# Kernel optimization log

Measured on AMD Instinct MI355X. Metric: run time of the kernel, lower is better.

Reference implementation:

```python
import jax, jax.numpy as jnp
import numpy as np

N = 50000      # nodes
E = 800000     # edges
D = 200        # in_dim = hid_dim
R = 230        # num_rels
B = 100        # bdd bases -> submat = D // B = 2
S = D // B     # submatrix size (2)


def setup_inputs() -> dict:
    key = jax.random.key(0)
    ks = jax.random.split(key, 16)
    node_feat = jax.random.normal(ks[0], (N, D), dtype=jnp.float32)
    dynamic_emb = jax.random.normal(ks[1], (N, 1, D), dtype=jnp.float32)
    src = jax.random.randint(ks[2], (E,), 0, N, dtype=jnp.int32)
    dst = jax.random.randint(ks[3], (E,), 0, N, dtype=jnp.int32)
    etypes = jax.random.randint(ks[4], (E,), 0, R, dtype=jnp.int32)
    # BDD relational weights per layer: [R, B, S, S]
    w1 = jax.random.normal(ks[5], (R, B, S, S), dtype=jnp.float32) * 0.1
    loop_w1 = jax.random.normal(ks[6], (D, D), dtype=jnp.float32) * 0.05
    b1 = jnp.zeros((D,), dtype=jnp.float32)
    w2 = jax.random.normal(ks[7], (R, B, S, S), dtype=jnp.float32) * 0.1
    loop_w2 = jax.random.normal(ks[8], (D, D), dtype=jnp.float32) * 0.05
    b2 = jnp.zeros((D,), dtype=jnp.float32)
    # single-layer vanilla RNN (tanh) params
    W_ih = jax.random.normal(ks[9], (D, D), dtype=jnp.float32) * 0.05
    W_hh = jax.random.normal(ks[10], (D, D), dtype=jnp.float32) * 0.05
    b_ih = jnp.zeros((D,), dtype=jnp.float32)
    b_hh = jnp.zeros((D,), dtype=jnp.float32)
    return {"node_feat": node_feat, "dynamic_emb": dynamic_emb,
            "src": src, "dst": dst, "etypes": etypes,
            "w1": w1, "loop_w1": loop_w1, "b1": b1,
            "w2": w2, "loop_w2": loop_w2, "b2": b2,
            "W_ih": W_ih, "W_hh": W_hh, "b_ih": b_ih, "b_hh": b_hh}


def _rel_graph_conv_bdd(x, src, dst, etypes, edge_norm, w, loop_w, b):
    # gather source feats and apply per-edge-type block-diagonal transform
    xs = x[src].reshape(E, B, S)                     # [E, B, S]
    msg = jnp.einsum('ebi,ebio->ebo', xs, w[etypes]) # [E, B, S]
    msg = msg.reshape(E, D) * edge_norm              # edge-norm scaling
    agg = jax.ops.segment_sum(msg, dst, num_segments=N)  # scatter-add to dst
    return agg + x @ loop_w + b                      # self-loop + bias


def reference(node_feat, dynamic_emb, src, dst, etypes,
              w1, loop_w1, b1, w2, loop_w2, b2,
              W_ih, W_hh, b_ih, b_hh):
    # edge_norm = dst node norm = 1 / in-degree
    deg = jax.ops.segment_sum(jnp.ones((E,), jnp.float32), dst, num_segments=N)
    node_norm = jnp.where(deg > 0, 1.0 / jnp.maximum(deg, 1.0), 0.0)
    edge_norm = node_norm[dst][:, None]              # [E, 1]

    # RGCN layer 1 (tanh activation), layer 2 (no activation); dropout=eval
    h = _rel_graph_conv_bdd(node_feat, src, dst, etypes, edge_norm, w1, loop_w1, b1)
    h = jnp.tanh(h)
    h = _rel_graph_conv_bdd(h, src, dst, etypes, edge_norm, w2, loop_w2, b2)

    # single-step vanilla RNN: hn = tanh(x W_ih^T + b_ih + h0 W_hh^T + b_hh)
    h0 = dynamic_emb[:, 0, :]                        # [N, D]
    hn = jnp.tanh(h @ W_ih.T + b_ih + h0 @ W_hh.T + b_hh)
    return hn[:, None, :]                            # [N, 1, D]
```

## Files before the change

kernel.cpp:

```cpp
#include <hip/hip_runtime.h>

#define N_NODES 50000
#define N_EDGES 800000
#define DIM     200
#define NBLK    100
#define NRELS   230
#define NB_SCAN 196
#define KPAD    224
#define KPN     256
#define NROWPAD 50048
#define NFRAG8  (8 * 14 * 64)
#define EPADMAX (N_EDGES + 3 * N_NODES + 16)
#define DUMMYROW 50000

typedef __attribute__((ext_vector_type(8)))  short short8;
typedef __attribute__((ext_vector_type(16))) float f32x16;

__device__ __forceinline__ unsigned short f2bf(float f) {
    unsigned u = __float_as_uint(f);
    u += 0x7fffu + ((u >> 16) & 1u);
    return (unsigned short)(u >> 16);
}

__device__ __forceinline__ float bflo(unsigned u) { return __uint_as_float(u << 16); }
__device__ __forceinline__ float bfhi(unsigned u) { return __uint_as_float(u & 0xffff0000u); }
__device__ __forceinline__ float b2f(unsigned short u) { return __uint_as_float((unsigned)u << 16); }

__device__ __forceinline__ float tanh_fast(float x) {
    float xa = fminf(fmaxf(x, -15.0f), 15.0f);
    float e = __expf(2.0f * xa);
    return (e - 1.0f) / (e + 1.0f);
}

__device__ __forceinline__ int uread(int v, int l) {
    return __builtin_amdgcn_readlane(v, l);
}

#if __has_builtin(__builtin_amdgcn_fdot2_f32_bf16)
typedef __bf16 bf16x2 __attribute__((ext_vector_type(2)));
__device__ __forceinline__ float dot2bf(unsigned a, unsigned b, float c) {
    return __builtin_amdgcn_fdot2_f32_bf16(
        __builtin_bit_cast(bf16x2, a), __builtin_bit_cast(bf16x2, b), c, false);
}
#define CMP4(XU, WU)                                                    \
    { m0 = dot2bf(XU.x, WU.x, m0); m1 = dot2bf(XU.x, WU.y, m1);         \
      m2 = dot2bf(XU.y, WU.z, m2); m3 = dot2bf(XU.y, WU.w, m3); }
#else
#define CMP4(XU, WU)                                                    \
    { float x0 = bflo(XU.x), x1 = bfhi(XU.x);                           \
      float x2 = bflo(XU.y), x3 = bfhi(XU.y);                           \
      m0 += x0 * bflo(WU.x) + x1 * bfhi(WU.x);                          \
      m1 += x0 * bflo(WU.y) + x1 * bfhi(WU.y);                          \
      m2 += x2 * bflo(WU.z) + x3 * bfhi(WU.z);                          \
      m3 += x2 * bflo(WU.w) + x3 * bfhi(WU.w); }
#endif

#define SWZ5(rr, off) ((unsigned)((rr) * 512 + (off)) ^ ((unsigned)((rr) & 15) << 4))
#define SWZH(rr, off) ((unsigned)((rr) * 256 + (off)) ^ ((unsigned)((rr) & 15) << 4))

#define FD_A (2 * NROWPAD * 28)
#define FD_B N_EDGES
#define FD_TOTAL (FD_A + FD_B)

__global__ void featdeg(const float* __restrict__ x, const float* __restrict__ de,
                        unsigned short* __restrict__ xb, unsigned short* __restrict__ h0b,
                        const int* __restrict__ dst, int* __restrict__ degi) {
    int idx = blockIdx.x * blockDim.x + threadIdx.x;
    if (idx < FD_A) {
        const int HALF = NROWPAD * 28;
        const float* src = (idx < HALF) ? x : de;
        unsigned short* o = (idx < HALF) ? xb : h0b;
        int j = (idx < HALF) ? idx : idx - HALF;
        int row = j / 28, c8 = j % 28;
        uint4 pk = {0, 0, 0, 0};
        if (row < N_NODES && c8 < 25) {
            const float* p = src + (size_t)row * DIM + c8 * 8;
            float4 a = *(const float4*)p;
            float4 b = *(const float4*)(p + 4);
            pk.x = (unsigned)f2bf(a.x) | ((unsigned)f2bf(a.y) << 16);
            pk.y = (unsigned)f2bf(a.z) | ((unsigned)f2bf(a.w) << 16);
            pk.z = (unsigned)f2bf(b.x) | ((unsigned)f2bf(b.y) << 16);
            pk.w = (unsigned)f2bf(b.z) | ((unsigned)f2bf(b.w) << 16);
        }
        *(uint4*)(o + (size_t)j * 8) = pk;
        return;
    }
    idx -= FD_A;
    if (idx < FD_B) atomicAdd(&degi[dst[idx]], 1);
}

#define PS_C (2 * NRELS * NBLK)
#define PS_D (3 * NFRAG8)
#define PS_E ((DIM + 1) * DIM)
#define PS_TOTAL (PS_C + PS_D + PS_E)

__global__ __launch_bounds__(256) void prep_small(
        const float* __restrict__ w1, const float* __restrict__ w2,
        unsigned short* __restrict__ w1b, unsigned short* __restrict__ w2b,
        const float* __restrict__ lw1, const float* __restrict__ wih,
        const float* __restrict__ whh,
        unsigned short* __restrict__ w1f, unsigned short* __restrict__ wihf,
        unsigned short* __restrict__ whhf,
        const float* __restrict__ lw2, const float* __restrict__ b2,
        const float* __restrict__ b_ih, const float* __restrict__ b_hh,
        float* __restrict__ Mt) {
    int idx = blockIdx.x * blockDim.x + threadIdx.x;
    if (idx < PS_C) {
        const int HALF = NRELS * NBLK;
        const float* w = (idx < HALF) ? w1 : w2;
        unsigned short* o = (idx < HALF) ? w1b : w2b;
        int j = (idx < HALF) ? idx : idx - HALF;
        float4 v = *(const float4*)(w + (size_t)j * 4);
        unsigned c0 = (unsigned)f2bf(v.x) | ((unsigned)f2bf(v.z) << 16);
        unsigned c1 = (unsigned)f2bf(v.y) | ((unsigned)f2bf(v.w) << 16);
        *(uint2*)(o + (size_t)j * 4) = make_uint2(c0, c1);
        return;
    }
    idx -= PS_C;
    if (idx < PS_D) {
        int sec = idx / NFRAG8, f = idx % NFRAG8;
        const float* w = (sec == 0) ? lw1 : (sec == 1) ? wih : whh;
        unsigned short* o = (sec == 0) ? w1f : (sec == 1) ? wihf : whhf;
        int l = f & 63;
        int ks = (f >> 6) % 14;
        int nt = f / (14 * 64);
        int n  = nt * 32 + (l & 31);
        int k0 = ks * 16 + (l >> 5) * 8;
        unsigned short v[8];
        #pragma unroll
        for (int j = 0; j < 8; ++j) {
            int k = k0 + j;
            float val = 0.0f;
            if (n < DIM && k < DIM)
                val = (sec == 0) ? w[k * DIM + n] : w[n * DIM + k];
            v[j] = f2bf(val);
        }
        *(uint4*)(o + (size_t)f * 8) = *(uint4*)v;
        return;
    }
    idx -= PS_D;
    if (idx < PS_E) {
        int k = idx / DIM, n = idx % DIM;
        const float* ar = (k < DIM) ? (lw2 + (size_t)k * DIM) : b2;
        const float* br = wih + (size_t)n * DIM;
        float s0 = 0.f, s1 = 0.f, s2 = 0.f, s3 = 0.f;
        #pragma unroll 5
        for (int q = 0; q < DIM; q += 4) {
            float4 a = *(const float4*)(ar + q);
            float4 b = *(const float4*)(br + q);
            s0 += a.x * b.x; s1 += a.y * b.y; s2 += a.z * b.z; s3 += a.w * b.w;
        }
        float s = (s0 + s1) + (s2 + s3);
        if (k == DIM) s += b_ih[n] + b_hh[n];
        Mt[idx] = s;
    }
}

__global__ __launch_bounds__(256) void scanA(const int* __restrict__ degi,
                                             int* __restrict__ pos, int* __restrict__ cur,
                                             int* __restrict__ bsum) {
    __shared__ int tmp[256];
    int t = threadIdx.x;
    int g = blockIdx.x * 256 + t;
    int d = (g < N_NODES) ? degi[g] : 0;
    int v = (d + 3) & ~3;
    tmp[t] = v;
    __syncthreads();
    for (int off = 1; off < 256; off <<= 1) {
        int xv = (t >= off) ? tmp[t - off] : 0;
        __syncthreads();
        tmp[t] += xv;
        __syncthreads();
    }
    if (g < N_NODES) { int e = tmp[t] - v; pos[g] = e; cur[g] = e; }
    if (t == 255) bsum[blockIdx.x] = tmp[255];
}

__global__ __launch_bounds__(256) void scanC2(int* __restrict__ pos, int* __restrict__ cur,
                                              const int* __restrict__ bsum) {
    __shared__ int tmp[256];
    __shared__ int excl[256];
    int t = threadIdx.x;
    int v = (t < NB_SCAN) ? bsum[t] : 0;
    tmp[t] = v;
    __syncthreads();
    for (int off = 1; off < 256; off <<= 1) {
        int xv = (t >= off) ? tmp[t - off] : 0;
        __syncthreads();
        tmp[t] += xv;
        __syncthreads();
    }
    excl[t] = tmp[t] - v;
    __syncthreads();
    int add = excl[blockIdx.x];
    int g = blockIdx.x * 256 + t;
    if (g < N_NODES) { pos[g] += add; cur[g] += add; }
}

#define M2_A N_EDGES
#define M2_B N_NODES
#define M2_C (NFRAG8 + KPN)
#define M2_TOTAL (M2_A + M2_B + M2_C)

__global__ __launch_bounds__(256) void mega2(
        const int* __restrict__ src, const int* __restrict__ dst,
        const int* __restrict__ et,
        int* __restrict__ cur, const int* __restrict__ pos,
        const int* __restrict__ degi, int* __restrict__ se,
        const float* __restrict__ Mt, unsigned short* __restrict__ Mf,
        float* __restrict__ biasv) {
    int idx = blockIdx.x * blockDim.x + threadIdx.x;
    if (idx < M2_A) {
        int d = dst[idx];
        int slot = atomicAdd(&cur[d], 1);
        se[slot] = src[idx] | (et[idx] << 16);
        return;
    }
    idx -= M2_A;
    if (idx < M2_B) {
        int d = degi[idx];
        if (d > 0) {
            int dp = (d + 3) & ~3;
            int start = pos[idx];
            for (int j = d; j < dp; ++j) se[start + j] = DUMMYROW;
        }
        return;
    }
    idx -= M2_B;
    if (idx < NFRAG8) {
        int l = idx & 63;
        int ks = (idx >> 6) % 14;
        int nt = idx / (14 * 64);
        int n  = nt * 32 + (l & 31);
        int k0 = ks * 16 + (l >> 5) * 8;
        unsigned short v[8];
        #pragma unroll
        for (int j = 0; j < 8; ++j) {
            int k = k0 + j;
            v[j] = f2bf((n < DIM && k < DIM) ? Mt[k * DIM + n] : 0.0f);
        }
        *(uint4*)(Mf + (size_t)idx * 8) = *(uint4*)v;
    } else if (idx < NFRAG8 + KPN) {
        int n = idx - NFRAG8;
        biasv[n] = (n < DIM) ? Mt[DIM * DIM + n] : 0.0f;
    }
}

#define GL(QQ, XU, WU)                                                  \
    { int p_ = uread(sv, (QQ)); int s_ = p_ & 0xffff; int r_ = p_ >> 16;\
      XU = *(const uint2*)(x  + (size_t)s_ * KPAD + xoff);              \
      WU = *(const uint4*)(wb + (size_t)r_ * (NBLK * 4) + woff); }

__global__ __launch_bounds__(256) void gatherB(
        const unsigned short* __restrict__ x,
        const int*   __restrict__ se,
        const int*   __restrict__ pstart,
        const int*   __restrict__ degi,
        const unsigned short* __restrict__ wb,
        unsigned short* __restrict__ agg) {
    int node = (blockIdx.x * blockDim.x + threadIdx.x) >> 6;
    int lane = threadIdx.x & 63;
    if (node >= N_NODES) return;
    int deg = __builtin_amdgcn_readfirstlane(degi[node]);
    const bool act = (lane < 50);
    int cl   = act ? lane : 49;
    int xoff = 4 * cl;
    int woff = 8 * cl;

    if (deg == 0) {
        if (lane < 56) *(uint2*)(agg + (size_t)node * KPAD + 4 * lane) = make_uint2(0u, 0u);
        return;
    }
    int start = __builtin_amdgcn_readfirstlane(pstart[node]);
    int degp  = (deg + 3) & ~3;

    float m0 = 0.f, m1 = 0.f, m2 = 0.f, m3 = 0.f;

    for (int base = 0; base < degp; base += 64) {
        int cnt = degp - base; if (cnt > 64) cnt = 64;
        int sv = se[start + base + (lane < cnt ? lane : cnt - 1)];

        uint2 X0, X1, X2, X3, Y0, Y1, Y2, Y3;
        uint4 W0, W1, W2, W3, V0, V1, V2, V3;
        GL(0, X0, W0); GL(1, X1, W1); GL(2, X2, W2); GL(3, X3, W3);

        for (int q = 0; q < cnt; q += 8) {
            bool l1 = (q + 4 < cnt);
            if (l1) { GL(q + 4, Y0, V0); GL(q + 5, Y1, V1); GL(q + 6, Y2, V2); GL(q + 7, Y3, V3); }
            CMP4(X0, W0); CMP4(X1, W1); CMP4(X2, W2); CMP4(X3, W3);
            if (!l1) break;
            bool l2 = (q + 8 < cnt);
            if (l2) { GL(q + 8, X0, W0); GL(q + 9, X1, W1); GL(q + 10, X2, W2); GL(q + 11, X3, W3); }
            CMP4(Y0, V0); CMP4(Y1, V1); CMP4(Y2, V2); CMP4(Y3, V3);
        }
    }
    float nrm = 1.0f / (float)deg;
    uint2 ov = make_uint2(0u, 0u);
    if (act) {
        ov.x = (unsigned)f2bf(m0 * nrm) | ((unsigned)f2bf(m1 * nrm) << 16);
        ov.y = (unsigned)f2bf(m2 * nrm) | ((unsigned)f2bf(m3 * nrm) << 16);
    }
    if (lane < 56) *(uint2*)(agg + (size_t)node * KPAD + 4 * lane) = ov;
}

__global__ __launch_bounds__(256) void gemm1_kernel(
        unsigned short* xb_hb,
        const unsigned short* __restrict__ agg1,
        const float* __restrict__ b1,
        const unsigned short* __restrict__ w1f) {
    __shared__ __align__(16) unsigned short s_a[32 * KPN];
    int row0 = blockIdx.x * 32;
    int tid = threadIdx.x;
    for (int i = tid; i < 32 * 32; i += 256) {
        int rr = i >> 5, ch = i & 31;
        uint4 v = {0, 0, 0, 0};
        if (ch < 28) v = *(const uint4*)(xb_hb + (size_t)(row0 + rr) * KPAD + ch * 8);
        *(uint4*)((char*)s_a + SWZ5(rr, ch * 16)) = v;
    }
    __syncthreads();

    int l = tid & 63, wv = tid >> 6;
    int rl = l & 31, hl = l >> 5;
    int ntlo = wv * 2;
    const unsigned short* wb = w1f + (size_t)(ntlo * 14) * 512 + l * 8;

    f32x16 acc0 = {}, acc1 = {};
    short8 aC  = *(const short8*)((const char*)s_a + SWZ5(rl, (hl * 8) * 2));
    short8 b0C = *(const short8*)(wb);
    short8 b1C = *(const short8*)(wb + 14 * 512);
    #pragma unroll
    for (int ks = 0; ks < 13; ++ks) {
        short8 aN = {}, b0N = {}, b1N = {};
        if (ks < 12) {
            aN  = *(const short8*)((const char*)s_a + SWZ5(rl, ((ks + 1) * 16 + hl * 8) * 2));
            b0N = *(const short8*)(wb + (ks + 1) * 512);
            b1N = *(const short8*)(wb + 14 * 512 + (ks + 1) * 512);
        }
        acc0 = __builtin_amdgcn_mfma_f32_32x32x16_bf16(aC, b0C, acc0, 0, 0, 0);
        acc1 = __builtin_amdgcn_mfma_f32_32x32x16_bf16(aC, b1C, acc1, 0, 0, 0);
        aC = aN; b0C = b0N; b1C = b1N;
    }
    __syncthreads();

    #pragma unroll
    for (int t = 0; t < 2; ++t) {
        f32x16 ac = t ? acc1 : acc0;
        int gc = (ntlo + t) * 32 + rl;
        if (gc >= KPAD) continue;
        float bias = (gc < DIM) ? b1[gc] : 0.0f;
        #pragma unroll
        for (int r = 0; r < 16; ++r) {
            int gr = row0 + (r & 3) + 8 * (r >> 2) + 4 * hl;
            float v = 0.0f;
            if (gc < DIM && gr < N_NODES)
                v = ac[r] + b2f(agg1[(size_t)gr * KPAD + gc]) + bias;
            xb_hb[(size_t)gr * KPAD + gc] = f2bf(tanh_fast(v));
        }
    }
}

__global__ __launch_bounds__(256) void gemm2_kernel(
        const unsigned short* __restrict__ hb,
        const unsigned short* __restrict__ aggp,
        const unsigned short* __restrict__ h0b,
        const unsigned short* __restrict__ Mf,
        const unsigned short* __restrict__ wihf,
        const unsigned short* __restrict__ whhf,
        const float* __restrict__ biasv,
        float* __restrict__ out) {
    __shared__ __align__(16) unsigned short s_h[32 * 128];
    __shared__ __align__(16) unsigned short s_g[32 * 128];
    __shared__ __align__(16) unsigned short s_e[32 * 128];
    int row0 = blockIdx.x * 32;
    int tid = threadIdx.x;
    int l = tid & 63, wv = tid >> 6;
    int rl = l & 31, hl = l >> 5;
    int ntlo = wv * 2;
    const unsigned short* pm = Mf   + (size_t)(ntlo * 14) * 512 + l * 8;
    const unsigned short* pi = wihf + (size_t)(ntlo * 14) * 512 + l * 8;
    const unsigned short* ph = whhf + (size_t)(ntlo * 14) * 512 + l * 8;

    f32x16 a0 = {}, a1 = {};

    for (int half = 0; half < 2; ++half) {
        for (int i = tid; i < 32 * 14; i += 256) {
            int rr = i / 14, ch = i % 14;
            size_t off = (size_t)(row0 + rr) * KPAD + (half * 14 + ch) * 8;
            unsigned sw = SWZH(rr, ch * 16);
            *(uint4*)((char*)s_h + sw) = *(const uint4*)(hb   + off);
            *(uint4*)((char*)s_g + sw) = *(const uint4*)(aggp + off);
            *(uint4*)((char*)s_e + sw) = *(const uint4*)(h0b  + off);
        }
        __syncthreads();

        const int kbase = half * 7;
        unsigned off0 = SWZH(rl, (hl * 8) * 2);
        short8 hC  = *(const short8*)((const char*)s_h + off0);
        short8 gC  = *(const short8*)((const char*)s_g + off0);
        short8 eC  = *(const short8*)((const char*)s_e + off0);
        short8 m0C = *(const short8*)(pm + kbase * 512);
        short8 m1C = *(const short8*)(pm + 14 * 512 + kbase * 512);
        short8 i0C = *(const short8*)(pi + kbase * 512);
        short8 i1C = *(const short8*)(pi + 14 * 512 + kbase * 512);
        short8 h0C = *(const short8*)(ph + kbase * 512);
        short8 h1C = *(const short8*)(ph + 14 * 512 + kbase * 512);
        #pragma unroll
        for (int ks = 0; ks < 7; ++ks) {
            short8 hN = {}, gN = {}, eN = {};
            short8 m0N = {}, m1N = {}, i0N = {}, i1N = {}, h0N = {}, h1N = {};
            if (ks < 6) {
                unsigned off = SWZH(rl, ((ks + 1) * 16 + hl * 8) * 2);
                hN  = *(const short8*)((const char*)s_h + off);
                gN  = *(const short8*)((const char*)s_g + off);
                eN  = *(const short8*)((const char*)s_e + off);
                int kg = kbase + ks + 1;
                m0N = *(const short8*)(pm + kg * 512);
                m1N = *(const short8*)(pm + 14 * 512 + kg * 512);
                i0N = *(const short8*)(pi + kg * 512);
                i1N = *(const short8*)(pi + 14 * 512 + kg * 512);
                h0N = *(const short8*)(ph + kg * 512);
                h1N = *(const short8*)(ph + 14 * 512 + kg * 512);
            }
            a0 = __builtin_amdgcn_mfma_f32_32x32x16_bf16(hC, m0C, a0, 0, 0, 0);
            a1 = __builtin_amdgcn_mfma_f32_32x32x16_bf16(hC, m1C, a1, 0, 0, 0);
            a0 = __builtin_amdgcn_mfma_f32_32x32x16_bf16(gC, i0C, a0, 0, 0, 0);
            a1 = __builtin_amdgcn_mfma_f32_32x32x16_bf16(gC, i1C, a1, 0, 0, 0);
            a0 = __builtin_amdgcn_mfma_f32_32x32x16_bf16(eC, h0C, a0, 0, 0, 0);
            a1 = __builtin_amdgcn_mfma_f32_32x32x16_bf16(eC, h1C, a1, 0, 0, 0);
            hC = hN; gC = gN; eC = eN;
            m0C = m0N; m1C = m1N; i0C = i0N; i1C = i1N; h0C = h0N; h1C = h1N;
        }
        __syncthreads();
    }

    #pragma unroll
    for (int t = 0; t < 2; ++t) {
        f32x16 oc = t ? a1 : a0;
        int gc = (ntlo + t) * 32 + rl;
        if (gc >= DIM) continue;
        float bias = biasv[gc];
        #pragma unroll
        for (int r = 0; r < 16; ++r) {
            int gr = row0 + (r & 3) + 8 * (r >> 2) + 4 * hl;
            if (gr < N_NODES)
                out[(size_t)gr * DIM + gc] = tanh_fast(oc[r] + bias);
        }
    }
}

extern "C" void kernel_launch(void* const* d_in, const int* in_sizes, int n_in,
                              void* d_out, int out_size, void* d_ws, size_t ws_size,
                              hipStream_t stream) {
    const float* node_feat = (const float*)d_in[0];
    const float* dyn_emb   = (const float*)d_in[1];
    const int*   src       = (const int*)  d_in[2];
    const int*   dst       = (const int*)  d_in[3];
    const int*   etypes    = (const int*)  d_in[4];
    const float* w1        = (const float*)d_in[5];
    const float* loop_w1   = (const float*)d_in[6];
    const float* b1        = (const float*)d_in[7];
    const float* w2        = (const float*)d_in[8];
    const float* loop_w2   = (const float*)d_in[9];
    const float* b2        = (const float*)d_in[10];
    const float* W_ih      = (const float*)d_in[11];
    const float* W_hh      = (const float*)d_in[12];
    const float* b_ih      = (const float*)d_in[13];
    const float* b_hh      = (const float*)d_in[14];
    float* out = (float*)d_out;

    int*   degi = (int*)d_ws;
    int*   pos  = degi + 51200;
    int*   cur  = pos  + 51200;
    int*   bsum = cur  + 51200;
    int*   se   = bsum + 256;
    unsigned short* aggp = (unsigned short*)(se + EPADMAX);
    unsigned short* hb   = aggp + (size_t)NROWPAD * KPAD;
    unsigned short* h0b  = hb   + (size_t)NROWPAD * KPAD;
    unsigned short* w1f  = h0b  + (size_t)NROWPAD * KPAD;
    unsigned short* wihf = w1f  + (size_t)NFRAG8 * 8;
    unsigned short* whhf = wihf + (size_t)NFRAG8 * 8;
    unsigned short* Mf   = whhf + (size_t)NFRAG8 * 8;
    unsigned short* w1b  = Mf   + (size_t)NFRAG8 * 8;
    unsigned short* w2b  = w1b  + (size_t)NRELS * NBLK * 4;
    float* biasv = (float*)(w2b + (size_t)NRELS * NBLK * 4);
    float* Mt    = biasv + KPN;

    hipMemsetAsync(degi, 0, 51200 * sizeof(int), stream);

    featdeg<<<(FD_TOTAL + 255) / 256, 256, 0, stream>>>(
        node_feat, dyn_emb, hb, h0b, dst, degi);
    prep_small<<<(PS_TOTAL + 255) / 256, 256, 0, stream>>>(
        w1, w2, w1b, w2b, loop_w1, W_ih, W_hh, w1f, wihf, whhf,
        loop_w2, b2, b_ih, b_hh, Mt);

    scanA<<<NB_SCAN, 256, 0, stream>>>(degi, pos, cur, bsum);
    scanC2<<<NB_SCAN, 256, 0, stream>>>(pos, cur, bsum);

    mega2<<<(M2_TOTAL + 255) / 256, 256, 0, stream>>>(
        src, dst, etypes, cur, pos, degi, se, Mt, Mf, biasv);

    gatherB<<<(N_NODES * 64 + 255) / 256, 256, 0, stream>>>(
        hb, se, pos, degi, w1b, aggp);
    gemm1_kernel<<<(N_NODES + 31) / 32, 256, 0, stream>>>(
        hb, aggp, b1, w1f);

    gatherB<<<(N_NODES * 64 + 255) / 256, 256, 0, stream>>>(
        hb, se, pos, degi, w2b, aggp);

    gemm2_kernel<<<(N_NODES + 31) / 32, 256, 0, stream>>>(
        hb, aggp, h0b, Mf, wihf, whhf, biasv, out);
}
```

Measured before the change: 333.5 us.

## Record per-edge rank from degree atomics to drop second atomic pass in CSR fill

The degree-count atomicAdd now saves its return value as a per-edge rank, so the CSR scatter in mega2 computes its slot as pos[dst]+rank with no second atomicAdd on a cursor array. Both edge loops now handle 8 edges per thread with vectorised int4 loads, and the feature bf16 conversion is split into its own kernel. The cur array and its writes in the scans are removed. This costs an extra 3.2 MB rank array written and read back, plus one more kernel launch.

```diff
diff --git a/kernel.cpp b/kernel.cpp
--- a/kernel.cpp
+++ b/kernel.cpp
@@ -58,35 +58,45 @@
 #define SWZ5(rr, off) ((unsigned)((rr) * 512 + (off)) ^ ((unsigned)((rr) & 15) << 4))
 #define SWZH(rr, off) ((unsigned)((rr) * 256 + (off)) ^ ((unsigned)((rr) & 15) << 4))
 
-#define FD_A (2 * NROWPAD * 28)
-#define FD_B N_EDGES
-#define FD_TOTAL (FD_A + FD_B)
-
-__global__ void featdeg(const float* __restrict__ x, const float* __restrict__ de,
-                        unsigned short* __restrict__ xb, unsigned short* __restrict__ h0b,
-                        const int* __restrict__ dst, int* __restrict__ degi) {
+__global__ void deg_rank(const int* __restrict__ dst, int* __restrict__ degi,
+                         int* __restrict__ rank) {
     int idx = blockIdx.x * blockDim.x + threadIdx.x;
-    if (idx < FD_A) {
-        const int HALF = NROWPAD * 28;
-        const float* src = (idx < HALF) ? x : de;
-        unsigned short* o = (idx < HALF) ? xb : h0b;
-        int j = (idx < HALF) ? idx : idx - HALF;
-        int row = j / 28, c8 = j % 28;
-        uint4 pk = {0, 0, 0, 0};
-        if (row < N_NODES && c8 < 25) {
-            const float* p = src + (size_t)row * DIM + c8 * 8;
-            float4 a = *(const float4*)p;
-            float4 b = *(const float4*)(p + 4);
-            pk.x = (unsigned)f2bf(a.x) | ((unsigned)f2bf(a.y) << 16);
-            pk.y = (unsigned)f2bf(a.z) | ((unsigned)f2bf(a.w) << 16);
-            pk.z = (unsigned)f2bf(b.x) | ((unsigned)f2bf(b.y) << 16);
-            pk.w = (unsigned)f2bf(b.z) | ((unsigned)f2bf(b.w) << 16);
-        }
-        *(uint4*)(o + (size_t)j * 8) = pk;
-        return;
-    }
-    idx -= FD_A;
-    if (idx < FD_B) atomicAdd(&degi[dst[idx]], 1);
+    if (idx >= N_EDGES / 8) return;
+    int e0 = idx * 8;
+    int4 da = *(const int4*)(dst + e0);
+    int4 db = *(const int4*)(dst + e0 + 4);
+    int r0 = atomicAdd(&degi[da.x], 1);
+    int r1 = atomicAdd(&degi[da.y], 1);
+    int r2 = atomicAdd(&degi[da.z], 1);
+    int r3 = atomicAdd(&degi[da.w], 1);
+    int r4 = atomicAdd(&degi[db.x], 1);
+    int r5 = atomicAdd(&degi[db.y], 1);
+    int r6 = atomicAdd(&degi[db.z], 1);
+    int r7 = atomicAdd(&degi[db.w], 1);
+    *(int4*)(rank + e0)     = make_int4(r0, r1, r2, r3);
+    *(int4*)(rank + e0 + 4) = make_int4(r4, r5, r6, r7);
+}
+
+__global__ void prep_feat2(const float* __restrict__ x, const float* __restrict__ de,
+                           unsigned short* __restrict__ xb, unsigned short* __restrict__ h0b) {
+    const int HALF = NROWPAD * 28;
+    int idx = blockIdx.x * blockDim.x + threadIdx.x;
+    if (idx >= 2 * HALF) return;
+    const float* src = (idx < HALF) ? x : de;
+    unsigned short* o = (idx < HALF) ? xb : h0b;
+    int j = (idx < HALF) ? idx : idx - HALF;
+    int row = j / 28, c8 = j % 28;
+    uint4 pk = {0, 0, 0, 0};
+    if (row < N_NODES && c8 < 25) {
+        const float* p = src + (size_t)row * DIM + c8 * 8;
+        float4 a = *(const float4*)p;
+        float4 b = *(const float4*)(p + 4);
+        pk.x = (unsigned)f2bf(a.x) | ((unsigned)f2bf(a.y) << 16);
+        pk.y = (unsigned)f2bf(a.z) | ((unsigned)f2bf(a.w) << 16);
+        pk.z = (unsigned)f2bf(b.x) | ((unsigned)f2bf(b.y) << 16);
+        pk.w = (unsigned)f2bf(b.z) | ((unsigned)f2bf(b.w) << 16);
+    }
+    *(uint4*)(o + (size_t)j * 8) = pk;
 }
 
 #define PS_C (2 * NRELS * NBLK)
@@ -157,7 +167,7 @@
 }
 
 __global__ __launch_bounds__(256) void scanA(const int* __restrict__ degi,
-                                             int* __restrict__ pos, int* __restrict__ cur,
+                                             int* __restrict__ pos,
                                              int* __restrict__ bsum) {
     __shared__ int tmp[256];
     int t = threadIdx.x;
@@ -172,11 +182,11 @@
         tmp[t] += xv;
         __syncthreads();
     }
-    if (g < N_NODES) { int e = tmp[t] - v; pos[g] = e; cur[g] = e; }
+    if (g < N_NODES) pos[g] = tmp[t] - v;
     if (t == 255) bsum[blockIdx.x] = tmp[255];
 }
 
-__global__ __launch_bounds__(256) void scanC2(int* __restrict__ pos, int* __restrict__ cur,
+__global__ __launch_bounds__(256) void scanC2(int* __restrict__ pos,
                                               const int* __restrict__ bsum) {
     __shared__ int tmp[256];
     __shared__ int excl[256];
@@ -194,26 +204,40 @@
     __syncthreads();
     int add = excl[blockIdx.x];
     int g = blockIdx.x * 256 + t;
-    if (g < N_NODES) { pos[g] += add; cur[g] += add; }
-}
-
-#define M2_A N_EDGES
+    if (g < N_NODES) pos[g] += add;
+}
+
+#define M2_A (N_EDGES / 8)
 #define M2_B N_NODES
 #define M2_C (NFRAG8 + KPN)
 #define M2_TOTAL (M2_A + M2_B + M2_C)
 
 __global__ __launch_bounds__(256) void mega2(
         const int* __restrict__ src, const int* __restrict__ dst,
-        const int* __restrict__ et,
-        int* __restrict__ cur, const int* __restrict__ pos,
-        const int* __restrict__ degi, int* __restrict__ se,
+        const int* __restrict__ et, const int* __restrict__ rank,
+        const int* __restrict__ pos, const int* __restrict__ degi,
+        int* __restrict__ se,
         const float* __restrict__ Mt, unsigned short* __restrict__ Mf,
         float* __restrict__ biasv) {
     int idx = blockIdx.x * blockDim.x + threadIdx.x;
     if (idx < M2_A) {
-        int d = dst[idx];
-        int slot = atomicAdd(&cur[d], 1);
-        se[slot] = src[idx] | (et[idx] << 16);
+        int e0 = idx * 8;
+        int4 da = *(const int4*)(dst + e0);
+        int4 db = *(const int4*)(dst + e0 + 4);
+        int4 sa = *(const int4*)(src + e0);
+        int4 sb = *(const int4*)(src + e0 + 4);
+        int4 ta = *(const int4*)(et + e0);
+        int4 tb = *(const int4*)(et + e0 + 4);
+        int4 ra = *(const int4*)(rank + e0);
+        int4 rb = *(const int4*)(rank + e0 + 4);
+        se[pos[da.x] + ra.x] = sa.x | (ta.x << 16);
+        se[pos[da.y] + ra.y] = sa.y | (ta.y << 16);
+        se[pos[da.z] + ra.z] = sa.z | (ta.z << 16);
+        se[pos[da.w] + ra.w] = sa.w | (ta.w << 16);
+        se[pos[db.x] + rb.x] = sb.x | (tb.x << 16);
+        se[pos[db.y] + rb.y] = sb.y | (tb.y << 16);
+        se[pos[db.z] + rb.z] = sb.z | (tb.z << 16);
+        se[pos[db.w] + rb.w] = sb.w | (tb.w << 16);
         return;
     }
     idx -= M2_A;
@@ -470,9 +494,9 @@
 
     int*   degi = (int*)d_ws;
     int*   pos  = degi + 51200;
-    int*   cur  = pos  + 51200;
-    int*   bsum = cur  + 51200;
-    int*   se   = bsum + 256;
+    int*   bsum = pos  + 51200;
+    int*   rank = bsum + 256;
+    int*   se   = rank + N_EDGES;
     unsigned short* aggp = (unsigned short*)(se + EPADMAX);
     unsigned short* hb   = aggp + (size_t)NROWPAD * KPAD;
     unsigned short* h0b  = hb   + (size_t)NROWPAD * KPAD;
@@ -487,17 +511,18 @@
 
     hipMemsetAsync(degi, 0, 51200 * sizeof(int), stream);
 
-    featdeg<<<(FD_TOTAL + 255) / 256, 256, 0, stream>>>(
-        node_feat, dyn_emb, hb, h0b, dst, degi);
+    deg_rank<<<(N_EDGES / 8 + 255) / 256, 256, 0, stream>>>(dst, degi, rank);
+    prep_feat2<<<(2 * NROWPAD * 28 + 255) / 256, 256, 0, stream>>>(
+        node_feat, dyn_emb, hb, h0b);
     prep_small<<<(PS_TOTAL + 255) / 256, 256, 0, stream>>>(
         w1, w2, w1b, w2b, loop_w1, W_ih, W_hh, w1f, wihf, whhf,
         loop_w2, b2, b_ih, b_hh, Mt);
 
-    scanA<<<NB_SCAN, 256, 0, stream>>>(degi, pos, cur, bsum);
-    scanC2<<<NB_SCAN, 256, 0, stream>>>(pos, cur, bsum);
+    scanA<<<NB_SCAN, 256, 0, stream>>>(degi, pos, bsum);
+    scanC2<<<NB_SCAN, 256, 0, stream>>>(pos, bsum);
 
     mega2<<<(M2_TOTAL + 255) / 256, 256, 0, stream>>>(
-        src, dst, etypes, cur, pos, degi, se, Mt, Mf, biasv);
+        src, dst, etypes, rank, pos, degi, se, Mt, Mf, biasv);
 
     gatherB<<<(N_NODES * 64 + 255) / 256, 256, 0, stream>>>(
         hb, se, pos, degi, w1b, aggp);
```

After: 292.5 us (median of 2 runs). 1.14x faster.
